# Kernel optimization log

Hardware: AMD Instinct MI355X
Metric: run time of the kernel (lower is better)

Reference implementation:

```python
import jax, jax.numpy as jnp
import numpy as np

N_NODES = 50000


def setup_inputs() -> dict:
    key = jax.random.key(0)
    k1, k2, k3, k4 = jax.random.split(key, 4)
    x = jax.random.normal(k1, (N_NODES, 128), dtype=jnp.float32)
    edge_index = jax.random.randint(k2, (2, 1600000), 0, N_NODES, dtype=jnp.int64)
    W1 = jax.random.normal(k3, (128, 256), dtype=jnp.float32) * (1.0 / np.sqrt(128))
    b1 = jnp.zeros((256,), dtype=jnp.float32)
    W2 = jax.random.normal(k4, (256, 1), dtype=jnp.float32) * (1.0 / np.sqrt(256))
    b2 = jnp.zeros((1,), dtype=jnp.float32)
    return {"x": x, "edge_index": edge_index, "W1": W1, "b1": b1, "W2": W2, "b2": b2}


def _gcn_conv(x, src, dst, norm, W, b, n_nodes):
    # PyG GCNConv: h = X W; out_i = sum_j norm_ij * h_j (+ self loop) + b
    h = x @ W                               # [N, F_out]
    msg = h[src] * norm[:, None]            # [E', F_out] gather + scale
    out = jax.ops.segment_sum(msg, dst, num_segments=n_nodes)  # scatter-add
    return out + b


def reference(x, edge_index, W1, b1, W2, b2):
    n = x.shape[0]
    loop = jnp.arange(n, dtype=edge_index.dtype)
    src = jnp.concatenate([edge_index[0], loop])   # add self loops
    dst = jnp.concatenate([edge_index[1], loop])
    # symmetric degree normalization on A + I
    deg = jax.ops.segment_sum(jnp.ones_like(dst, dtype=x.dtype), dst, num_segments=n)
    dis = jnp.where(deg > 0, jax.lax.rsqrt(deg), 0.0)
    norm = dis[src] * dis[dst]                     # [E']
    h = jax.nn.relu(_gcn_conv(x, src, dst, norm, W1, b1, n))
    return _gcn_conv(h, src, dst, norm, W2, b2, n)
```

## Files before the change

kernel.cpp:

```cpp
#include <hip/hip_runtime.h>


#define EPB_LOG 12
#define EPB (1 << EPB_LOG)
#define BW_LOG 7
#define BW (1 << BW_LOG)
#define MAXBUCK 512
#define SCAN_TILE 2048

typedef __attribute__((ext_vector_type(8))) short bf16x8;
typedef __attribute__((ext_vector_type(4))) float f32x4;

__device__ inline unsigned short f2bf(float f) {
    unsigned int b = __float_as_uint(f);
    unsigned int r = b + 0x7FFFu + ((b >> 16) & 1u);
    return (unsigned short)(r >> 16);
}
__device__ inline float bf_lo(unsigned int u) { return __uint_as_float(u << 16); }
__device__ inline float bf_hi(unsigned int u) { return __uint_as_float(u & 0xFFFF0000u); }

__global__ void k_init(const int* __restrict__ edges, int* __restrict__ flag,
                       int* __restrict__ cnt, int* __restrict__ btot_raw,
                       int* __restrict__ row_start, int n, long long E) {
    int i = blockIdx.x * blockDim.x + threadIdx.x;
    if (i < n) cnt[i] = 0;
    if (i < MAXBUCK) btot_raw[i] = 0;
    if (i == 0) row_start[n] = (int)E;
    if (blockIdx.x == 0 && threadIdx.x < 64) {
        int v = edges[2 * threadIdx.x + 1];
        unsigned long long b = __ballot(v != 0);
        if (threadIdx.x == 0) flag[0] = b ? 1 : 2;
    }
}

__global__ __launch_bounds__(128) void k_prep_w(const float* __restrict__ W1,
        unsigned short* __restrict__ w1t) {
    int n = blockIdx.x;
    int k = threadIdx.x;
    w1t[n * 128 + k] = f2bf(W1[k * 256 + n]);
}

__global__ __launch_bounds__(256) void k_prep_xs(const float* __restrict__ x,
        const float* __restrict__ dis, unsigned short* __restrict__ xs, int n) {
    int i = blockIdx.x * 256 + threadIdx.x;
    if (i >= n * 32) return;
    float dsc = dis[i >> 5];
    float4 v = ((const float4*)x)[i];
    ushort4 o;
    o.x = f2bf(v.x * dsc); o.y = f2bf(v.y * dsc);
    o.z = f2bf(v.z * dsc); o.w = f2bf(v.w * dsc);
    ((ushort4*)xs)[i] = o;
}

__global__ __launch_bounds__(256) void k_bucket_count(
        const int* __restrict__ edges, const int* __restrict__ flag,
        int* __restrict__ btot_raw, long long E, int nbuck) {
    __shared__ int bins[MAXBUCK];
    int sb = blockIdx.x, t = threadIdx.x;
    for (int i = t; i < nbuck; i += 256) bins[i] = 0;
    __syncthreads();
    int stride = flag[0];
    long long base = (long long)sb << EPB_LOG;
    long long rem = E - base;
    int nE = (rem < (long long)EPB) ? (int)rem : EPB;
    for (int i = t; i < nE; i += 256) {
        int d = edges[(E + base + i) * stride];
        atomicAdd(&bins[d >> BW_LOG], 1);
    }
    __syncthreads();
    for (int i = t; i < nbuck; i += 256)
        if (bins[i]) atomicAdd(&btot_raw[i], bins[i]);
}

__global__ __launch_bounds__(256) void k_btot_scan(
        const int* __restrict__ btot_raw, int* __restrict__ btot,
        int* __restrict__ curg, int nbuck) {
    __shared__ int ws4[4];
    int t = threadIdx.x;
    int c4 = (nbuck + 255) >> 8;
    int lo = t * c4;
    int hi = lo + c4; if (hi > nbuck) hi = nbuck;
    if (lo > nbuck) lo = nbuck;
    int vals[2];
    int local = 0;
    for (int i = lo; i < hi; ++i) { vals[i - lo] = btot_raw[i]; local += vals[i - lo]; }
    int lane = t & 63, w = t >> 6;
    int inc = local;
    for (int off = 1; off < 64; off <<= 1) {
        int u = __shfl_up(inc, off, 64);
        if (lane >= off) inc += u;
    }
    if (lane == 63) ws4[w] = inc;
    __syncthreads();
    int woff = 0;
    for (int i = 0; i < w; ++i) woff += ws4[i];
    int ex = woff + inc - local;
    for (int i = lo; i < hi; ++i) {
        btot[i] = ex; curg[i] = ex;
        ex += vals[i - lo];
    }
}

__global__ __launch_bounds__(256) void k_partition(
        const int* __restrict__ edges, const int* __restrict__ flag,
        int* __restrict__ curg, unsigned int* __restrict__ part,
        long long E, int nbuck) {
    __shared__ unsigned int stage[EPB];
    __shared__ int bins[MAXBUCK];
    __shared__ int lcur[MAXBUCK];
    __shared__ int gbase[MAXBUCK];
    __shared__ int ws4[4];
    int sb = blockIdx.x, t = threadIdx.x;
    int stride = flag[0];
    long long base = (long long)sb << EPB_LOG;
    long long rem = E - base;
    int nE = (rem < (long long)EPB) ? (int)rem : EPB;
    for (int i = t; i < nbuck; i += 256) bins[i] = 0;
    __syncthreads();
    for (int i = t; i < nE; i += 256) {
        int d = edges[(E + base + i) * stride];
        atomicAdd(&bins[d >> BW_LOG], 1);
    }
    __syncthreads();
    for (int i = t; i < nbuck; i += 256) {
        int c = bins[i];
        gbase[i] = c ? atomicAdd(&curg[i], c) : 0;
    }
    int c4 = (nbuck + 255) >> 8;
    int lo = t * c4;
    int hi = lo + c4; if (hi > nbuck) hi = nbuck;
    if (lo > nbuck) lo = nbuck;
    int vals[2];
    int local = 0;
    for (int i = lo; i < hi; ++i) { vals[i - lo] = bins[i]; local += vals[i - lo]; }
    int lane = t & 63, w = t >> 6;
    int inc = local;
    for (int off = 1; off < 64; off <<= 1) {
        int u = __shfl_up(inc, off, 64);
        if (lane >= off) inc += u;
    }
    if (lane == 63) ws4[w] = inc;
    __syncthreads();
    int woff = 0;
    for (int i = 0; i < w; ++i) woff += ws4[i];
    int ex = woff + inc - local;
    for (int i = lo; i < hi; ++i) {
        bins[i] = ex;
        lcur[i] = ex;
        ex += vals[i - lo];
    }
    __syncthreads();
    for (int i = t; i < nE; i += 256) {
        int s = edges[(base + i) * stride];
        int d = edges[(E + base + i) * stride];
        int b = d >> BW_LOG;
        int p = atomicAdd(&lcur[b], 1);
        stage[p] = ((unsigned int)s << 16) | (unsigned int)d;
    }
    __syncthreads();
    for (int i = t; i < nE; i += 256) {
        unsigned int pk = stage[i];
        int b = (int)(pk & 0xFFFFu) >> BW_LOG;
        part[gbase[b] + (i - bins[b])] = pk;
    }
}

__global__ __launch_bounds__(256) void k_deg_dis(
        const unsigned int* __restrict__ part, const int* __restrict__ btot,
        int* __restrict__ row_start, float* __restrict__ dis,
        int nbuck, int n, long long E) {
    __shared__ int c128[BW];
    __shared__ int ws4[4];
    int b = blockIdx.x, t = threadIdx.x;
    if (t < BW) c128[t] = 0;
    __syncthreads();
    int start = btot[b];
    int endp = (b + 1 < nbuck) ? btot[b + 1] : (int)E;
    for (int i = start + t; i < endp; i += 256)
        atomicAdd(&c128[part[i] & (BW - 1)], 1);
    __syncthreads();
    int deg = (t < BW) ? c128[t] : 0;
    int lane = t & 63, w = t >> 6;
    int inc = deg;
    for (int off = 1; off < 64; off <<= 1) {
        int u = __shfl_up(inc, off, 64);
        if (lane >= off) inc += u;
    }
    if (lane == 63) ws4[w] = inc;
    __syncthreads();
    int woff = 0;
    for (int i = 0; i < w; ++i) woff += ws4[i];
    int ex = woff + inc - deg;
    if (t < BW) {
        int d = (b << BW_LOG) + t;
        if (d < n) {
            row_start[d] = start + ex;
            dis[d] = rsqrtf((float)deg + 1.0f);
        }
    }
}

__global__ __launch_bounds__(256) void k_scatter2(
        const unsigned int* __restrict__ part, const int* __restrict__ btot,
        const int* __restrict__ row_start, int* __restrict__ csr_src,
        int nbuck, long long E) {
    __shared__ int cur[BW];
    int b = blockIdx.x, t = threadIdx.x;
    if (t < BW) cur[t] = 0;
    __syncthreads();
    int start = btot[b];
    int endp = (b + 1 < nbuck) ? btot[b + 1] : (int)E;
    for (int i = start + t; i < endp; i += 256) {
        unsigned int pk = part[i];
        int d = (int)(pk & 0xFFFFu);
        int r = atomicAdd(&cur[d & (BW - 1)], 1);
        csr_src[row_start[d] + r] = (int)(pk >> 16);
    }
}

__global__ __launch_bounds__(256) void k_agg(
        const unsigned short* __restrict__ xs, const int* __restrict__ csr_src,
        const int* __restrict__ row_start, const float* __restrict__ dis,
        unsigned short* __restrict__ aggh, int n) {
    int wid  = (blockIdx.x * blockDim.x + threadIdx.x) >> 6;
    int lane = threadIdx.x & 63;
    if (wid >= n) return;
    int start = row_start[wid], end = row_start[wid + 1];
    unsigned int self = ((const unsigned int*)(xs + (size_t)wid * 128))[lane];
    float acc0 = bf_lo(self);
    float acc1 = bf_hi(self);
    int e = start;
    for (; e + 7 < end; e += 8) {
        int s0 = csr_src[e],     s1 = csr_src[e + 1];
        int s2 = csr_src[e + 2], s3 = csr_src[e + 3];
        int s4 = csr_src[e + 4], s5 = csr_src[e + 5];
        int s6 = csr_src[e + 6], s7 = csr_src[e + 7];
        unsigned int v0 = ((const unsigned int*)(xs + (size_t)s0 * 128))[lane];
        unsigned int v1 = ((const unsigned int*)(xs + (size_t)s1 * 128))[lane];
        unsigned int v2 = ((const unsigned int*)(xs + (size_t)s2 * 128))[lane];
        unsigned int v3 = ((const unsigned int*)(xs + (size_t)s3 * 128))[lane];
        unsigned int v4 = ((const unsigned int*)(xs + (size_t)s4 * 128))[lane];
        unsigned int v5 = ((const unsigned int*)(xs + (size_t)s5 * 128))[lane];
        unsigned int v6 = ((const unsigned int*)(xs + (size_t)s6 * 128))[lane];
        unsigned int v7 = ((const unsigned int*)(xs + (size_t)s7 * 128))[lane];
        acc0 += bf_lo(v0); acc1 += bf_hi(v0);
        acc0 += bf_lo(v1); acc1 += bf_hi(v1);
        acc0 += bf_lo(v2); acc1 += bf_hi(v2);
        acc0 += bf_lo(v3); acc1 += bf_hi(v3);
        acc0 += bf_lo(v4); acc1 += bf_hi(v4);
        acc0 += bf_lo(v5); acc1 += bf_hi(v5);
        acc0 += bf_lo(v6); acc1 += bf_hi(v6);
        acc0 += bf_lo(v7); acc1 += bf_hi(v7);
    }
    for (; e < end; ++e) {
        int s0 = csr_src[e];
        unsigned int v0 = ((const unsigned int*)(xs + (size_t)s0 * 128))[lane];
        acc0 += bf_lo(v0); acc1 += bf_hi(v0);
    }
    float dn = dis[wid];
    unsigned int pack = (unsigned int)f2bf(acc0 * dn) | ((unsigned int)f2bf(acc1 * dn) << 16);
    ((unsigned int*)(aggh + (size_t)wid * 128))[lane] = pack;
}

__global__ __launch_bounds__(256) void k_mm(
        const unsigned short* __restrict__ aggh, const unsigned short* __restrict__ w1t,
        const float* __restrict__ b1, const float* __restrict__ W2,
        const float* __restrict__ dis, float* __restrict__ svs, int n) {
    int wave = threadIdx.x >> 6;
    int lane = threadIdx.x & 63;
    int m    = lane & 15;
    int quad = lane >> 4;
    int node0 = blockIdx.x * 64 + wave * 16;

    bf16x8 afrag[4];
    const unsigned short* arow = aggh + (size_t)(node0 + m) * 128 + quad * 8;
#pragma unroll
    for (int ks = 0; ks < 4; ++ks)
        afrag[ks] = *(const bf16x8*)(arow + ks * 32);

    float p0 = 0.f, p1 = 0.f, p2 = 0.f, p3 = 0.f;
#pragma unroll 1
    for (int t = 0; t < 16; ++t) {
        const unsigned short* brow = w1t + (size_t)(t * 16 + m) * 128 + quad * 8;
        f32x4 acc = {0.f, 0.f, 0.f, 0.f};
#pragma unroll
        for (int ks = 0; ks < 4; ++ks) {
            bf16x8 bfrag = *(const bf16x8*)(brow + ks * 32);
            acc = __builtin_amdgcn_mfma_f32_16x16x32_bf16(afrag[ks], bfrag, acc, 0, 0, 0);
        }
        int col = t * 16 + m;
        float bb = b1[col], w2 = W2[col];
        float h0 = acc[0] + bb, h1 = acc[1] + bb, h2 = acc[2] + bb, h3 = acc[3] + bb;
        p0 += (h0 > 0.f ? h0 : 0.f) * w2;
        p1 += (h1 > 0.f ? h1 : 0.f) * w2;
        p2 += (h2 > 0.f ? h2 : 0.f) * w2;
        p3 += (h3 > 0.f ? h3 : 0.f) * w2;
    }
#pragma unroll
    for (int off = 1; off < 16; off <<= 1) {
        p0 += __shfl_xor(p0, off, 64);
        p1 += __shfl_xor(p1, off, 64);
        p2 += __shfl_xor(p2, off, 64);
        p3 += __shfl_xor(p3, off, 64);
    }
    if (m == 0) {
        int nb = node0 + quad * 4;
        if (nb + 0 < n) svs[nb + 0] = p0 * dis[nb + 0];
        if (nb + 1 < n) svs[nb + 1] = p1 * dis[nb + 1];
        if (nb + 2 < n) svs[nb + 2] = p2 * dis[nb + 2];
        if (nb + 3 < n) svs[nb + 3] = p3 * dis[nb + 3];
    }
}

__global__ __launch_bounds__(256) void k_out(
        const float* __restrict__ svs, const int* __restrict__ csr_src,
        const int* __restrict__ row_start, const float* __restrict__ dis,
        const float* __restrict__ b2, float* __restrict__ out, int n) {
    int wid  = (blockIdx.x * blockDim.x + threadIdx.x) >> 6;
    int lane = threadIdx.x & 63;
    if (wid >= n) return;
    int start = row_start[wid], end = row_start[wid + 1];
    float acc = 0.f;
    for (int e = start + lane; e < end; e += 64)
        acc += svs[csr_src[e]];
    for (int off = 32; off; off >>= 1) acc += __shfl_down(acc, off, 64);
    if (lane == 0)
        out[wid] = dis[wid] * (acc + svs[wid]) + b2[0];
}

__global__ void k_count_slow(const int* __restrict__ edges, const int* __restrict__ flag,
                             int* __restrict__ cnt, int* __restrict__ posi, long long E) {
    long long e = (long long)blockIdx.x * blockDim.x + threadIdx.x;
    if (e >= E) return;
    int stride = flag[0];
    int d = edges[(E + e) * stride];
    posi[e] = atomicAdd(&cnt[d], 1);
}
__global__ __launch_bounds__(256) void k_scan_partial(
        const int* __restrict__ cnt, int* __restrict__ bsum, int n) {
    int t = threadIdx.x;
    int idx = blockIdx.x * SCAN_TILE + t * 8;
    int s = 0;
#pragma unroll
    for (int j = 0; j < 8; ++j) { int i = idx + j; if (i < n) s += cnt[i]; }
    for (int off = 32; off; off >>= 1) s += __shfl_down(s, off, 64);
    __shared__ int ws[4];
    if ((t & 63) == 0) ws[t >> 6] = s;
    __syncthreads();
    if (t == 0) bsum[blockIdx.x] = ws[0] + ws[1] + ws[2] + ws[3];
}
__global__ void k_scan_tops(int* __restrict__ bsum, int nb) {
    int t = threadIdx.x;
    int w = (t < nb) ? bsum[t] : 0;
    int v = w;
    for (int off = 1; off < 64; off <<= 1) {
        int u = __shfl_up(v, off, 64);
        if (t >= off) v += u;
    }
    if (t < nb) bsum[t] = v - w;
}
__global__ __launch_bounds__(256) void k_scan_apply(
        const int* __restrict__ cnt, const int* __restrict__ bsum,
        int* __restrict__ row_start, float* __restrict__ dis, int n) {
    int t = threadIdx.x;
    int lane = t & 63, w = t >> 6;
    int idx = blockIdx.x * SCAN_TILE + t * 8;
    int vals[8];
    int s = 0;
#pragma unroll
    for (int j = 0; j < 8; ++j) { int i = idx + j; vals[j] = (i < n) ? cnt[i] : 0; s += vals[j]; }
    int inc = s;
    for (int off = 1; off < 64; off <<= 1) {
        int u = __shfl_up(inc, off, 64);
        if (lane >= off) inc += u;
    }
    __shared__ int wsum[4];
    if (lane == 63) wsum[w] = inc;
    __syncthreads();
    int woff = 0;
    for (int i = 0; i < w; ++i) woff += wsum[i];
    int ex = bsum[blockIdx.x] + woff + inc - s;
#pragma unroll
    for (int j = 0; j < 8; ++j) {
        int i = idx + j;
        if (i < n) {
            row_start[i] = ex;
            dis[i] = rsqrtf((float)vals[j] + 1.0f);
            ex += vals[j];
        }
    }
    if (idx <= n && n < idx + 8) row_start[n] = ex;
}
__global__ void k_scatter_slow(const int* __restrict__ edges, const int* __restrict__ flag,
                               const int* __restrict__ row_start, const int* __restrict__ posi,
                               int* __restrict__ csr_src, long long E) {
    long long e = (long long)blockIdx.x * blockDim.x + threadIdx.x;
    if (e >= E) return;
    int stride = flag[0];
    int s = edges[e * stride];
    int d = edges[(E + e) * stride];
    csr_src[row_start[d] + posi[e]] = s;
}

extern "C" void kernel_launch(void* const* d_in, const int* in_sizes, int n_in,
                              void* d_out, int out_size, void* d_ws, size_t ws_size,
                              hipStream_t stream) {
    const float* x  = (const float*)d_in[0];
    const int*   ei = (const int*)d_in[1];
    const float* W1 = (const float*)d_in[2];
    const float* b1 = (const float*)d_in[3];
    const float* W2 = (const float*)d_in[4];
    const float* b2 = (const float*)d_in[5];
    float* out = (float*)d_out;

    const int N = in_sizes[0] / 128;
    const long long E = in_sizes[1] / 2;
    const int nsb = (int)((E + EPB - 1) >> EPB_LOG);
    const int nbuck = (N + BW - 1) >> BW_LOG;

    char* ws = (char*)d_ws;
    size_t off = 0;
    auto take = [&](size_t bytes) -> char* {
        char* p = ws + off;
        off = (off + bytes + 255) & ~(size_t)255;
        return p;
    };
    int*            flag     = (int*)take(4);
    int*            cnt      = (int*)take((size_t)N * 4);
    int*            rs       = (int*)take((size_t)(N + 1) * 4);
    float*          dis      = (float*)take((size_t)N * 4);
    float*          svs      = (float*)take((size_t)N * 4);
    int*            bsum     = (int*)take(64 * 4);
    int*            btot_raw = (int*)take(MAXBUCK * 4);
    int*            btot     = (int*)take(MAXBUCK * 4);
    int*            curg     = (int*)take(MAXBUCK * 4);
    unsigned int*   part     = (unsigned int*)take((size_t)E * 4);
    int*            csr_src  = (int*)take((size_t)E * 4);
    unsigned short* xs       = (unsigned short*)take((size_t)N * 128 * 2);
    unsigned short* w1t      = (unsigned short*)take((size_t)256 * 128 * 2);
    unsigned short* aggh     = (unsigned short*)take((size_t)(N + 64) * 128 * 2);

    int nb_n  = (N + 255) / 256;
    int nb_e  = (int)((E + 255) / 256);
    int nb_s  = (N + SCAN_TILE - 1) / SCAN_TILE;
    int nb_x  = (N * 32 + 255) / 256;
    int nb_mm = (N + 63) / 64;

    bool fast = (N < 65536);

    k_init   <<<nb_n, 256, 0, stream>>>(ei, flag, cnt, btot_raw, rs, N, E);
    k_prep_w <<<256, 128, 0, stream>>>(W1, w1t);
    if (fast) {
        k_bucket_count<<<nsb, 256, 0, stream>>>(ei, flag, btot_raw, E, nbuck);
        k_btot_scan   <<<1, 256, 0, stream>>>(btot_raw, btot, curg, nbuck);
        k_partition   <<<nsb, 256, 0, stream>>>(ei, flag, curg, part, E, nbuck);
        k_deg_dis     <<<nbuck, 256, 0, stream>>>(part, btot, rs, dis, nbuck, N, E);
        k_prep_xs     <<<nb_x, 256, 0, stream>>>(x, dis, xs, N);
        k_scatter2    <<<nbuck, 256, 0, stream>>>(part, btot, rs, csr_src, nbuck, E);
    } else {
        k_count_slow  <<<nb_e, 256, 0, stream>>>(ei, flag, cnt, (int*)part, E);
        k_scan_partial<<<nb_s, 256, 0, stream>>>(cnt, bsum, N);
        k_scan_tops   <<<1, 64, 0, stream>>>(bsum, nb_s);
        k_scan_apply  <<<nb_s, 256, 0, stream>>>(cnt, bsum, rs, dis, N);
        k_prep_xs     <<<nb_x, 256, 0, stream>>>(x, dis, xs, N);
        k_scatter_slow<<<nb_e, 256, 0, stream>>>(ei, flag, rs, (const int*)part, csr_src, E);
    }
    k_agg<<<(N + 3) / 4, 256, 0, stream>>>(xs, csr_src, rs, dis, aggh, N);
    k_mm <<<nb_mm, 256, 0, stream>>>(aggh, w1t, b1, W2, dis, svs, N);
    k_out<<<(N + 3) / 4, 256, 0, stream>>>(svs, csr_src, rs, dis, b2, out, N);
}
```

Before: 244.9 us.

## Fuse CSR build, x prep, aggregation and matmul kernels to cut launches

Merges several kernels on the fast path. Stride detection and W1 conversion move into the bucket-count kernel. Degree, CSR scatter and x scaling become one per-bucket kernel, and neighbour aggregation now feeds the MFMA matmul through LDS instead of a global aggh buffer. The partition kernel caches dst in LDS so edges are not reloaded. The aim is fewer launches and less global traffic. The cost is that half the waves in the agg-mm block sit idle during the matmul, and the larger LDS and block size may reduce occupancy.

Result: faster. 237.8 us (-2.9%).

```diff
diff --git a/kernel.cpp b/kernel.cpp
--- a/kernel.cpp
+++ b/kernel.cpp
@@ -7,6 +7,7 @@
 #define BW (1 << BW_LOG)
 #define MAXBUCK 512
 #define SCAN_TILE 2048
+#define AMSTRIDE 136
 
 typedef __attribute__((ext_vector_type(8))) short bf16x8;
 typedef __attribute__((ext_vector_type(4))) float f32x4;
@@ -19,48 +20,33 @@
 __device__ inline float bf_lo(unsigned int u) { return __uint_as_float(u << 16); }
 __device__ inline float bf_hi(unsigned int u) { return __uint_as_float(u & 0xFFFF0000u); }
 
-__global__ void k_init(const int* __restrict__ edges, int* __restrict__ flag,
-                       int* __restrict__ cnt, int* __restrict__ btot_raw,
-                       int* __restrict__ row_start, int n, long long E) {
-    int i = blockIdx.x * blockDim.x + threadIdx.x;
-    if (i < n) cnt[i] = 0;
-    if (i < MAXBUCK) btot_raw[i] = 0;
-    if (i == 0) row_start[n] = (int)E;
-    if (blockIdx.x == 0 && threadIdx.x < 64) {
-        int v = edges[2 * threadIdx.x + 1];
-        unsigned long long b = __ballot(v != 0);
-        if (threadIdx.x == 0) flag[0] = b ? 1 : 2;
-    }
-}
-
-__global__ __launch_bounds__(128) void k_prep_w(const float* __restrict__ W1,
-        unsigned short* __restrict__ w1t) {
-    int n = blockIdx.x;
-    int k = threadIdx.x;
-    w1t[n * 128 + k] = f2bf(W1[k * 256 + n]);
-}
-
-__global__ __launch_bounds__(256) void k_prep_xs(const float* __restrict__ x,
-        const float* __restrict__ dis, unsigned short* __restrict__ xs, int n) {
-    int i = blockIdx.x * 256 + threadIdx.x;
-    if (i >= n * 32) return;
-    float dsc = dis[i >> 5];
-    float4 v = ((const float4*)x)[i];
-    ushort4 o;
-    o.x = f2bf(v.x * dsc); o.y = f2bf(v.y * dsc);
-    o.z = f2bf(v.z * dsc); o.w = f2bf(v.w * dsc);
-    ((ushort4*)xs)[i] = o;
-}
-
-__global__ __launch_bounds__(256) void k_bucket_count(
-        const int* __restrict__ edges, const int* __restrict__ flag,
-        int* __restrict__ btot_raw, long long E, int nbuck) {
+__device__ inline int detect_stride(const int* edges, int t, int* sh) {
+    if (t < 64) {
+        int v = edges[2 * t + 1];
+        unsigned long long bb = __ballot(v != 0);
+        if (t == 0) *sh = bb ? 1 : 2;
+    }
+    __syncthreads();
+    return *sh;
+}
+
+
+__global__ __launch_bounds__(256) void k_count(
+        const int* __restrict__ edges, const float* __restrict__ W1,
+        unsigned short* __restrict__ w1t, int* __restrict__ btot_raw,
+        long long E, int nbuck, int nsb) {
+    int b = blockIdx.x, t = threadIdx.x;
+    if (b >= nsb) {
+        int row = (b - nsb) * 2 + (t >> 7);
+        int k = t & 127;
+        w1t[row * 128 + k] = f2bf(W1[k * 256 + row]);
+        return;
+    }
     __shared__ int bins[MAXBUCK];
-    int sb = blockIdx.x, t = threadIdx.x;
+    __shared__ int sh;
     for (int i = t; i < nbuck; i += 256) bins[i] = 0;
-    __syncthreads();
-    int stride = flag[0];
-    long long base = (long long)sb << EPB_LOG;
+    int stride = detect_stride(edges, t, &sh);
+    long long base = (long long)b << EPB_LOG;
     long long rem = E - base;
     int nE = (rem < (long long)EPB) ? (int)rem : EPB;
     for (int i = t; i < nE; i += 256) {
@@ -102,30 +88,27 @@
 }
 
 __global__ __launch_bounds__(256) void k_partition(
-        const int* __restrict__ edges, const int* __restrict__ flag,
-        int* __restrict__ curg, unsigned int* __restrict__ part,
-        long long E, int nbuck) {
+        const int* __restrict__ edges, int* __restrict__ curg,
+        unsigned int* __restrict__ part, long long E, int nbuck) {
     __shared__ unsigned int stage[EPB];
+    __shared__ unsigned short dst16[EPB];
     __shared__ int bins[MAXBUCK];
     __shared__ int lcur[MAXBUCK];
     __shared__ int gbase[MAXBUCK];
     __shared__ int ws4[4];
+    __shared__ int sh;
     int sb = blockIdx.x, t = threadIdx.x;
-    int stride = flag[0];
+    for (int i = t; i < nbuck; i += 256) bins[i] = 0;
+    int stride = detect_stride(edges, t, &sh);
     long long base = (long long)sb << EPB_LOG;
     long long rem = E - base;
     int nE = (rem < (long long)EPB) ? (int)rem : EPB;
-    for (int i = t; i < nbuck; i += 256) bins[i] = 0;
-    __syncthreads();
     for (int i = t; i < nE; i += 256) {
         int d = edges[(E + base + i) * stride];
+        dst16[i] = (unsigned short)d;
         atomicAdd(&bins[d >> BW_LOG], 1);
     }
     __syncthreads();
-    for (int i = t; i < nbuck; i += 256) {
-        int c = bins[i];
-        gbase[i] = c ? atomicAdd(&curg[i], c) : 0;
-    }
     int c4 = (nbuck + 255) >> 8;
     int lo = t * c4;
     int hi = lo + c4; if (hi > nbuck) hi = nbuck;
@@ -133,6 +116,11 @@
     int vals[2];
     int local = 0;
     for (int i = lo; i < hi; ++i) { vals[i - lo] = bins[i]; local += vals[i - lo]; }
+    for (int i = t; i < nbuck; i += 256) {
+        int c = bins[i];
+        gbase[i] = c ? atomicAdd(&curg[i], c) : 0;
+    }
+    __syncthreads();
     int lane = t & 63, w = t >> 6;
     int inc = local;
     for (int off = 1; off < 64; off <<= 1) {
@@ -152,7 +140,7 @@
     __syncthreads();
     for (int i = t; i < nE; i += 256) {
         int s = edges[(base + i) * stride];
-        int d = edges[(E + base + i) * stride];
+        int d = dst16[i];
         int b = d >> BW_LOG;
         int p = atomicAdd(&lcur[b], 1);
         stage[p] = ((unsigned int)s << 16) | (unsigned int)d;
@@ -165,12 +153,15 @@
     }
 }
 
-__global__ __launch_bounds__(256) void k_deg_dis(
+__global__ __launch_bounds__(256) void k_build_csr(
         const unsigned int* __restrict__ part, const int* __restrict__ btot,
-        int* __restrict__ row_start, float* __restrict__ dis,
-        int nbuck, int n, long long E) {
+        const float* __restrict__ x, int* __restrict__ row_start,
+        float* __restrict__ dis, int* __restrict__ csr_src,
+        unsigned short* __restrict__ xs, int nbuck, int n, long long E) {
     __shared__ int c128[BW];
-    __shared__ int ws4[4];
+    __shared__ int lcur[BW];
+    __shared__ float dld[BW];
+    __shared__ int ws2[2];
     int b = blockIdx.x, t = threadIdx.x;
     if (t < BW) c128[t] = 0;
     __syncthreads();
@@ -179,116 +170,121 @@
     for (int i = start + t; i < endp; i += 256)
         atomicAdd(&c128[part[i] & (BW - 1)], 1);
     __syncthreads();
+    int lane = t & 63, w = t >> 6;
     int deg = (t < BW) ? c128[t] : 0;
-    int lane = t & 63, w = t >> 6;
     int inc = deg;
     for (int off = 1; off < 64; off <<= 1) {
         int u = __shfl_up(inc, off, 64);
         if (lane >= off) inc += u;
     }
-    if (lane == 63) ws4[w] = inc;
-    __syncthreads();
-    int woff = 0;
-    for (int i = 0; i < w; ++i) woff += ws4[i];
-    int ex = woff + inc - deg;
+    if (t < BW && lane == 63) ws2[w] = inc;
+    __syncthreads();
     if (t < BW) {
+        int ex = inc - deg + ((w == 1) ? ws2[0] : 0);
+        lcur[t] = ex;
         int d = (b << BW_LOG) + t;
         if (d < n) {
             row_start[d] = start + ex;
-            dis[d] = rsqrtf((float)deg + 1.0f);
+            float dv = rsqrtf((float)deg + 1.0f);
+            dis[d] = dv;
+            dld[t] = dv;
         }
     }
-}
-
-__global__ __launch_bounds__(256) void k_scatter2(
-        const unsigned int* __restrict__ part, const int* __restrict__ btot,
-        const int* __restrict__ row_start, int* __restrict__ csr_src,
-        int nbuck, long long E) {
-    __shared__ int cur[BW];
-    int b = blockIdx.x, t = threadIdx.x;
-    if (t < BW) cur[t] = 0;
-    __syncthreads();
-    int start = btot[b];
-    int endp = (b + 1 < nbuck) ? btot[b + 1] : (int)E;
+    if (b == nbuck - 1 && t == 0) row_start[n] = (int)E;
+    __syncthreads();
     for (int i = start + t; i < endp; i += 256) {
         unsigned int pk = part[i];
-        int d = (int)(pk & 0xFFFFu);
-        int r = atomicAdd(&cur[d & (BW - 1)], 1);
-        csr_src[row_start[d] + r] = (int)(pk >> 16);
-    }
-}
-
-__global__ __launch_bounds__(256) void k_agg(
+        int r = atomicAdd(&lcur[pk & (BW - 1)], 1);
+        csr_src[start + r] = (int)(pk >> 16);
+    }
+    int d0 = b << BW_LOG;
+    for (int idx = t; idx < BW * 32; idx += 256) {
+        int node = d0 + (idx >> 5);
+        if (node >= n) break;
+        float dv = dld[idx >> 5];
+        float4 v = ((const float4*)x)[(size_t)node * 32 + (idx & 31)];
+        ushort4 o;
+        o.x = f2bf(v.x * dv); o.y = f2bf(v.y * dv);
+        o.z = f2bf(v.z * dv); o.w = f2bf(v.w * dv);
+        ((ushort4*)xs)[(size_t)node * 32 + (idx & 31)] = o;
+    }
+}
+
+__global__ __launch_bounds__(512) void k_agg_mm(
         const unsigned short* __restrict__ xs, const int* __restrict__ csr_src,
-        const int* __restrict__ row_start, const float* __restrict__ dis,
-        unsigned short* __restrict__ aggh, int n) {
-    int wid  = (blockIdx.x * blockDim.x + threadIdx.x) >> 6;
-    int lane = threadIdx.x & 63;
-    if (wid >= n) return;
-    int start = row_start[wid], end = row_start[wid + 1];
-    unsigned int self = ((const unsigned int*)(xs + (size_t)wid * 128))[lane];
-    float acc0 = bf_lo(self);
-    float acc1 = bf_hi(self);
-    int e = start;
-    for (; e + 7 < end; e += 8) {
-        int s0 = csr_src[e],     s1 = csr_src[e + 1];
-        int s2 = csr_src[e + 2], s3 = csr_src[e + 3];
-        int s4 = csr_src[e + 4], s5 = csr_src[e + 5];
-        int s6 = csr_src[e + 6], s7 = csr_src[e + 7];
-        unsigned int v0 = ((const unsigned int*)(xs + (size_t)s0 * 128))[lane];
-        unsigned int v1 = ((const unsigned int*)(xs + (size_t)s1 * 128))[lane];
-        unsigned int v2 = ((const unsigned int*)(xs + (size_t)s2 * 128))[lane];
-        unsigned int v3 = ((const unsigned int*)(xs + (size_t)s3 * 128))[lane];
-        unsigned int v4 = ((const unsigned int*)(xs + (size_t)s4 * 128))[lane];
-        unsigned int v5 = ((const unsigned int*)(xs + (size_t)s5 * 128))[lane];
-        unsigned int v6 = ((const unsigned int*)(xs + (size_t)s6 * 128))[lane];
-        unsigned int v7 = ((const unsigned int*)(xs + (size_t)s7 * 128))[lane];
-        acc0 += bf_lo(v0); acc1 += bf_hi(v0);
-        acc0 += bf_lo(v1); acc1 += bf_hi(v1);
-        acc0 += bf_lo(v2); acc1 += bf_hi(v2);
-        acc0 += bf_lo(v3); acc1 += bf_hi(v3);
-        acc0 += bf_lo(v4); acc1 += bf_hi(v4);
-        acc0 += bf_lo(v5); acc1 += bf_hi(v5);
-        acc0 += bf_lo(v6); acc1 += bf_hi(v6);
-        acc0 += bf_lo(v7); acc1 += bf_hi(v7);
-    }
-    for (; e < end; ++e) {
-        int s0 = csr_src[e];
-        unsigned int v0 = ((const unsigned int*)(xs + (size_t)s0 * 128))[lane];
-        acc0 += bf_lo(v0); acc1 += bf_hi(v0);
-    }
-    float dn = dis[wid];
-    unsigned int pack = (unsigned int)f2bf(acc0 * dn) | ((unsigned int)f2bf(acc1 * dn) << 16);
-    ((unsigned int*)(aggh + (size_t)wid * 128))[lane] = pack;
-}
-
-__global__ __launch_bounds__(256) void k_mm(
-        const unsigned short* __restrict__ aggh, const unsigned short* __restrict__ w1t,
-        const float* __restrict__ b1, const float* __restrict__ W2,
-        const float* __restrict__ dis, float* __restrict__ svs, int n) {
-    int wave = threadIdx.x >> 6;
-    int lane = threadIdx.x & 63;
-    int m    = lane & 15;
+        const int* __restrict__ rs, const float* __restrict__ dis,
+        const unsigned short* __restrict__ w1t, const float* __restrict__ b1,
+        const float* __restrict__ W2, float* __restrict__ svs, int n) {
+    __shared__ short am[64 * AMSTRIDE];
+    int t = threadIdx.x;
+    int lane = t & 63, w = t >> 6;
+    int blk = blockIdx.x;
+    const unsigned int* xsu = (const unsigned int*)xs;
+#pragma unroll 1
+    for (int jj = 0; jj < 8; ++jj) {
+        int r = w * 8 + jj;
+        int node = blk * 64 + r;
+        unsigned int pack = 0;
+        if (node < n) {
+            int start = rs[node], end = rs[node + 1];
+            unsigned int self = xsu[((size_t)node << 6) + lane];
+            float a0 = bf_lo(self), a1 = bf_hi(self);
+            int e = start;
+            for (; e + 7 < end; e += 8) {
+                int s0 = csr_src[e],     s1 = csr_src[e + 1];
+                int s2 = csr_src[e + 2], s3 = csr_src[e + 3];
+                int s4 = csr_src[e + 4], s5 = csr_src[e + 5];
+                int s6 = csr_src[e + 6], s7 = csr_src[e + 7];
+                unsigned int v0 = xsu[((size_t)s0 << 6) + lane];
+                unsigned int v1 = xsu[((size_t)s1 << 6) + lane];
+                unsigned int v2 = xsu[((size_t)s2 << 6) + lane];
+                unsigned int v3 = xsu[((size_t)s3 << 6) + lane];
+                unsigned int v4 = xsu[((size_t)s4 << 6) + lane];
+                unsigned int v5 = xsu[((size_t)s5 << 6) + lane];
+                unsigned int v6 = xsu[((size_t)s6 << 6) + lane];
+                unsigned int v7 = xsu[((size_t)s7 << 6) + lane];
+                a0 += bf_lo(v0); a1 += bf_hi(v0);
+                a0 += bf_lo(v1); a1 += bf_hi(v1);
+                a0 += bf_lo(v2); a1 += bf_hi(v2);
+                a0 += bf_lo(v3); a1 += bf_hi(v3);
+                a0 += bf_lo(v4); a1 += bf_hi(v4);
+                a0 += bf_lo(v5); a1 += bf_hi(v5);
+                a0 += bf_lo(v6); a1 += bf_hi(v6);
+                a0 += bf_lo(v7); a1 += bf_hi(v7);
+            }
+            for (; e < end; ++e) {
+                int s0 = csr_src[e];
+                unsigned int v0 = xsu[((size_t)s0 << 6) + lane];
+                a0 += bf_lo(v0); a1 += bf_hi(v0);
+            }
+            float dn = dis[node];
+            pack = (unsigned int)f2bf(a0 * dn) | ((unsigned int)f2bf(a1 * dn) << 16);
+        }
+        *(unsigned int*)&am[r * AMSTRIDE + 2 * lane] = pack;
+    }
+    __syncthreads();
+    if (w >= 4) return;
+    int m = lane & 15;
     int quad = lane >> 4;
-    int node0 = blockIdx.x * 64 + wave * 16;
+    int node0 = blk * 64 + w * 16;
 
     bf16x8 afrag[4];
-    const unsigned short* arow = aggh + (size_t)(node0 + m) * 128 + quad * 8;
+    const short* arow = &am[(w * 16 + m) * AMSTRIDE + quad * 8];
 #pragma unroll
     for (int ks = 0; ks < 4; ++ks)
         afrag[ks] = *(const bf16x8*)(arow + ks * 32);
 
     float p0 = 0.f, p1 = 0.f, p2 = 0.f, p3 = 0.f;
 #pragma unroll 1
-    for (int t = 0; t < 16; ++t) {
-        const unsigned short* brow = w1t + (size_t)(t * 16 + m) * 128 + quad * 8;
+    for (int tt = 0; tt < 16; ++tt) {
+        const unsigned short* brow = w1t + (size_t)(tt * 16 + m) * 128 + quad * 8;
         f32x4 acc = {0.f, 0.f, 0.f, 0.f};
 #pragma unroll
         for (int ks = 0; ks < 4; ++ks) {
             bf16x8 bfrag = *(const bf16x8*)(brow + ks * 32);
             acc = __builtin_amdgcn_mfma_f32_16x16x32_bf16(afrag[ks], bfrag, acc, 0, 0, 0);
         }
-        int col = t * 16 + m;
+        int col = tt * 16 + m;
         float bb = b1[col], w2 = W2[col];
         float h0 = acc[0] + bb, h1 = acc[1] + bb, h2 = acc[2] + bb, h3 = acc[3] + bb;
         p0 += (h0 > 0.f ? h0 : 0.f) * w2;
@@ -328,6 +324,32 @@
         out[wid] = dis[wid] * (acc + svs[wid]) + b2[0];
 }
 
+__global__ void k_init(const int* __restrict__ edges, int* __restrict__ flag,
+                       int* __restrict__ cnt, int n) {
+    int i = blockIdx.x * blockDim.x + threadIdx.x;
+    if (i < n) cnt[i] = 0;
+    if (blockIdx.x == 0 && threadIdx.x < 64) {
+        int v = edges[2 * threadIdx.x + 1];
+        unsigned long long b = __ballot(v != 0);
+        if (threadIdx.x == 0) flag[0] = b ? 1 : 2;
+    }
+}
+__global__ __launch_bounds__(128) void k_prep_w(const float* __restrict__ W1,
+        unsigned short* __restrict__ w1t) {
+    int nn = blockIdx.x, k = threadIdx.x;
+    w1t[nn * 128 + k] = f2bf(W1[k * 256 + nn]);
+}
+__global__ __launch_bounds__(256) void k_prep_xs(const float* __restrict__ x,
+        const float* __restrict__ dis, unsigned short* __restrict__ xs, int n) {
+    int i = blockIdx.x * 256 + threadIdx.x;
+    if (i >= n * 32) return;
+    float dsc = dis[i >> 5];
+    float4 v = ((const float4*)x)[i];
+    ushort4 o;
+    o.x = f2bf(v.x * dsc); o.y = f2bf(v.y * dsc);
+    o.z = f2bf(v.z * dsc); o.w = f2bf(v.w * dsc);
+    ((ushort4*)xs)[i] = o;
+}
 __global__ void k_count_slow(const int* __restrict__ edges, const int* __restrict__ flag,
                              int* __restrict__ cnt, int* __restrict__ posi, long long E) {
     long long e = (long long)blockIdx.x * blockDim.x + threadIdx.x;
@@ -400,6 +422,70 @@
     int s = edges[e * stride];
     int d = edges[(E + e) * stride];
     csr_src[row_start[d] + posi[e]] = s;
+}
+__global__ __launch_bounds__(256) void k_agg(
+        const unsigned short* __restrict__ xs, const int* __restrict__ csr_src,
+        const int* __restrict__ row_start, const float* __restrict__ dis,
+        unsigned short* __restrict__ aggh, int n) {
+    int wid  = (blockIdx.x * blockDim.x + threadIdx.x) >> 6;
+    int lane = threadIdx.x & 63;
+    if (wid >= n) return;
+    int start = row_start[wid], end = row_start[wid + 1];
+    unsigned int self = ((const unsigned int*)xs)[((size_t)wid << 6) + lane];
+    float a0 = bf_lo(self), a1 = bf_hi(self);
+    for (int e = start; e < end; ++e) {
+        int s0 = csr_src[e];
+        unsigned int v0 = ((const unsigned int*)xs)[((size_t)s0 << 6) + lane];
+        a0 += bf_lo(v0); a1 += bf_hi(v0);
+    }
+    float dn = dis[wid];
+    unsigned int pack = (unsigned int)f2bf(a0 * dn) | ((unsigned int)f2bf(a1 * dn) << 16);
+    ((unsigned int*)aggh)[((size_t)wid << 6) + lane] = pack;
+}
+__global__ __launch_bounds__(256) void k_mm(
+        const unsigned short* __restrict__ aggh, const unsigned short* __restrict__ w1t,
+        const float* __restrict__ b1, const float* __restrict__ W2,
+        const float* __restrict__ dis, float* __restrict__ svs, int n) {
+    int wave = threadIdx.x >> 6;
+    int lane = threadIdx.x & 63;
+    int m = lane & 15, quad = lane >> 4;
+    int node0 = blockIdx.x * 64 + wave * 16;
+    bf16x8 afrag[4];
+    const unsigned short* arow = aggh + (size_t)(node0 + m) * 128 + quad * 8;
+#pragma unroll
+    for (int ks = 0; ks < 4; ++ks) afrag[ks] = *(const bf16x8*)(arow + ks * 32);
+    float p0 = 0.f, p1 = 0.f, p2 = 0.f, p3 = 0.f;
+#pragma unroll 1
+    for (int tt = 0; tt < 16; ++tt) {
+        const unsigned short* brow = w1t + (size_t)(tt * 16 + m) * 128 + quad * 8;
+        f32x4 acc = {0.f, 0.f, 0.f, 0.f};
+#pragma unroll
+        for (int ks = 0; ks < 4; ++ks) {
+            bf16x8 bfrag = *(const bf16x8*)(brow + ks * 32);
+            acc = __builtin_amdgcn_mfma_f32_16x16x32_bf16(afrag[ks], bfrag, acc, 0, 0, 0);
+        }
+        int col = tt * 16 + m;
+        float bb = b1[col], w2 = W2[col];
+        float h0 = acc[0] + bb, h1 = acc[1] + bb, h2 = acc[2] + bb, h3 = acc[3] + bb;
+        p0 += (h0 > 0.f ? h0 : 0.f) * w2;
+        p1 += (h1 > 0.f ? h1 : 0.f) * w2;
+        p2 += (h2 > 0.f ? h2 : 0.f) * w2;
+        p3 += (h3 > 0.f ? h3 : 0.f) * w2;
+    }
+#pragma unroll
+    for (int off = 1; off < 16; off <<= 1) {
+        p0 += __shfl_xor(p0, off, 64);
+        p1 += __shfl_xor(p1, off, 64);
+        p2 += __shfl_xor(p2, off, 64);
+        p3 += __shfl_xor(p3, off, 64);
+    }
+    if (m == 0) {
+        int nb = node0 + quad * 4;
+        if (nb + 0 < n) svs[nb + 0] = p0 * dis[nb + 0];
+        if (nb + 1 < n) svs[nb + 1] = p1 * dis[nb + 1];
+        if (nb + 2 < n) svs[nb + 2] = p2 * dis[nb + 2];
+        if (nb + 3 < n) svs[nb + 3] = p3 * dis[nb + 3];
+    }
 }
 
 extern "C" void kernel_launch(void* const* d_in, const int* in_sizes, int n_in,
@@ -444,28 +530,30 @@
     int nb_e  = (int)((E + 255) / 256);
     int nb_s  = (N + SCAN_TILE - 1) / SCAN_TILE;
     int nb_x  = (N * 32 + 255) / 256;
-    int nb_mm = (N + 63) / 64;
+    int nb_am = (N + 63) / 64;
 
     bool fast = (N < 65536);
 
-    k_init   <<<nb_n, 256, 0, stream>>>(ei, flag, cnt, btot_raw, rs, N, E);
-    k_prep_w <<<256, 128, 0, stream>>>(W1, w1t);
     if (fast) {
-        k_bucket_count<<<nsb, 256, 0, stream>>>(ei, flag, btot_raw, E, nbuck);
-        k_btot_scan   <<<1, 256, 0, stream>>>(btot_raw, btot, curg, nbuck);
-        k_partition   <<<nsb, 256, 0, stream>>>(ei, flag, curg, part, E, nbuck);
-        k_deg_dis     <<<nbuck, 256, 0, stream>>>(part, btot, rs, dis, nbuck, N, E);
-        k_prep_xs     <<<nb_x, 256, 0, stream>>>(x, dis, xs, N);
-        k_scatter2    <<<nbuck, 256, 0, stream>>>(part, btot, rs, csr_src, nbuck, E);
+        hipMemsetAsync(btot_raw, 0, (size_t)nbuck * 4, stream);
+        k_count    <<<nsb + 128, 256, 0, stream>>>(ei, W1, w1t, btot_raw, E, nbuck, nsb);
+        k_btot_scan<<<1, 256, 0, stream>>>(btot_raw, btot, curg, nbuck);
+        k_partition<<<nsb, 256, 0, stream>>>(ei, curg, part, E, nbuck);
+        k_build_csr<<<nbuck, 256, 0, stream>>>(part, btot, x, rs, dis, csr_src,
+                                               xs, nbuck, N, E);
+        k_agg_mm   <<<nb_am, 512, 0, stream>>>(xs, csr_src, rs, dis, w1t, b1, W2, svs, N);
+        k_out      <<<(N + 3) / 4, 256, 0, stream>>>(svs, csr_src, rs, dis, b2, out, N);
     } else {
+        k_init        <<<nb_n, 256, 0, stream>>>(ei, flag, cnt, N);
+        k_prep_w      <<<256, 128, 0, stream>>>(W1, w1t);
         k_count_slow  <<<nb_e, 256, 0, stream>>>(ei, flag, cnt, (int*)part, E);
         k_scan_partial<<<nb_s, 256, 0, stream>>>(cnt, bsum, N);
         k_scan_tops   <<<1, 64, 0, stream>>>(bsum, nb_s);
         k_scan_apply  <<<nb_s, 256, 0, stream>>>(cnt, bsum, rs, dis, N);
         k_prep_xs     <<<nb_x, 256, 0, stream>>>(x, dis, xs, N);
         k_scatter_slow<<<nb_e, 256, 0, stream>>>(ei, flag, rs, (const int*)part, csr_src, E);
-    }
-    k_agg<<<(N + 3) / 4, 256, 0, stream>>>(xs, csr_src, rs, dis, aggh, N);
-    k_mm <<<nb_mm, 256, 0, stream>>>(aggh, w1t, b1, W2, dis, svs, N);
-    k_out<<<(N + 3) / 4, 256, 0, stream>>>(svs, csr_src, rs, dis, b2, out, N);
-}
+        k_agg         <<<(N + 3) / 4, 256, 0, stream>>>(xs, csr_src, rs, dis, aggh, N);
+        k_mm          <<<(N + 63) / 64, 256, 0, stream>>>(aggh, w1t, b1, W2, dis, svs, N);
+        k_out         <<<(N + 3) / 4, 256, 0, stream>>>(svs, csr_src, rs, dis, b2, out, N);
+    }
+}
```
